# Kernel optimization log

Hardware: AMD Instinct MI355X
Metric: run time of the kernel (lower is better)

The kernel has to match this reference:

```python
import jax, jax.numpy as jnp
import numpy as np

N = 500_000   # total nodes
B = 500       # number of graphs
C = 128       # channels


def setup_inputs() -> dict:
    key = jax.random.key(0)
    ks = jax.random.split(key, 10)
    node_embeddings = jax.random.normal(ks[0], (N, C), dtype=jnp.float32)
    latent_embeddings = jax.random.normal(ks[1], (B, C), dtype=jnp.float32)
    groups = jnp.sort(jax.random.randint(ks[2], (N,), 0, B)).astype(jnp.int32)
    # params (PyTorch Linear stored here as [in, out] matrices; same math)
    s = 1.0 / np.sqrt(C)
    attn_w = jax.random.normal(ks[3], (C, 1), dtype=jnp.float32) * s  # xavier-ish
    w_w = jax.random.normal(ks[4], (C, 1), dtype=jnp.float32) * s
    w_b = jnp.zeros((1,), dtype=jnp.float32)
    f1_w = jax.random.normal(ks[5], (C, C), dtype=jnp.float32) * s
    f1_b = jnp.zeros((C,), dtype=jnp.float32)
    f2_w = jax.random.normal(ks[6], (C, 1), dtype=jnp.float32) * s
    f2_b = jnp.zeros((1,), dtype=jnp.float32)
    return {
        "node_embeddings": node_embeddings,
        "latent_embeddings": latent_embeddings,
        "attn_w": attn_w, "w_w": w_w, "w_b": w_b,
        "f1_w": f1_w, "f1_b": f1_b, "f2_w": f2_w, "f2_b": f2_b,
        "groups": groups, "num_segments": B,
    }


def reference(node_embeddings, latent_embeddings, attn_w, w_w, w_b,
              f1_w, f1_b, f2_w, f2_b, groups, num_segments):
    # gather per-node context (faithful to original: indexes node table by graph id)
    ctx = node_embeddings[groups]            # [N, C]
    lat = latent_embeddings[groups]          # [N, C]
    alpha = jax.nn.sigmoid(ctx @ w_w + w_b)  # [N, 1]
    f_out = jax.nn.relu(lat @ f1_w + f1_b) @ f2_w + f2_b  # [N, 1]
    attn = alpha * f_out + (1.0 - alpha) * attn_w.T       # [N, C]
    scores = jnp.sum(node_embeddings * attn, axis=1, keepdims=True)  # [N, 1]
    scores = jnp.exp(scores - jnp.max(scores, axis=0, keepdims=True))
    denom = jax.ops.segment_sum(scores, groups, num_segments=num_segments)[groups]
    scores = scores / denom
    graph_embeddings = jax.ops.segment_sum(node_embeddings * scores, groups,
                                           num_segments=num_segments)  # [B, C]
    return graph_embeddings
```

## Files before the change

### kernel.cpp

```cpp
#include <hip/hip_runtime.h>
#include <math.h>

#define C 128
#define NW 16

typedef float f32x4 __attribute__((ext_vector_type(4)));

__global__ void k_prep(const int* __restrict__ groups, int n, int b, int nbb,
                       const float* __restrict__ node,
                       const float* __restrict__ latent,
                       const float* __restrict__ attn_w,
                       const float* __restrict__ w_w,
                       const float* __restrict__ w_b,
                       const float* __restrict__ f1_w,
                       const float* __restrict__ f1_b,
                       const float* __restrict__ f2_w,
                       const float* __restrict__ f2_b,
                       int* __restrict__ start, float* __restrict__ attnv) {
    __shared__ float lds_lat[C];
    __shared__ float red[4];

    if ((int)blockIdx.x < nbb) {
        int i = blockIdx.x * blockDim.x + threadIdx.x;
        if (i >= n) return;
        int g = groups[i];
        int gp = (i == 0) ? -1 : groups[i - 1];
        for (int gg = gp + 1; gg <= g; ++gg) start[gg] = i;
        if (i == n - 1)
            for (int gg = g + 1; gg <= b; ++gg) start[gg] = n;
        return;
    }

    const int g = blockIdx.x - nbb;
    const int tid = threadIdx.x;
    const int lane = tid & 63;
    const int wv = tid >> 6;

    if (tid < C) lds_lat[tid] = latent[(size_t)g * C + tid];
    __syncthreads();
    if (tid < C) {
        float ap = node[(size_t)g * C + tid] * w_w[tid];
        float h0 = 0.f, h1 = 0.f;
        #pragma unroll 8
        for (int in = 0; in < C / 2; ++in)
            h0 = fmaf(lds_lat[in], f1_w[in * C + tid], h0);
        #pragma unroll 8
        for (int in = C / 2; in < C; ++in)
            h1 = fmaf(lds_lat[in], f1_w[in * C + tid], h1);
        float h = fmaxf(h0 + h1 + f1_b[tid], 0.f);
        float fp = h * f2_w[tid];
        #pragma unroll
        for (int off = 32; off >= 1; off >>= 1) {
            ap += __shfl_xor(ap, off);
            fp += __shfl_xor(fp, off);
        }
        if (lane == 0) { red[wv * 2] = ap; red[wv * 2 + 1] = fp; }
    }
    __syncthreads();
    if (tid < C) {
        float a_sum = red[0] + red[2];
        float f_sum = red[1] + red[3];
        float alpha = 1.f / (1.f + __expf(-(a_sum + w_b[0])));
        float fout = f_sum + f2_b[0];
        attnv[(size_t)g * C + tid] = alpha * fout + (1.f - alpha) * attn_w[tid];
    }
}

__global__ __launch_bounds__(1024, 8)
void k_attn(const float* __restrict__ node,
            const float* __restrict__ attnv,
            const int* __restrict__ start,
            float* __restrict__ out) {
    const int g = blockIdx.x;
    const int tid = threadIdx.x;
    const int lane = tid & 63;
    const int wv = tid >> 6;

    __shared__ float wacc[NW][C];
    __shared__ float wm[NW], wd[NW];

    const int lo = start[g], hi = start[g + 1];

    const int half = lane >> 5;
    const int cl = lane & 31;
    const f32x4 av = *(const f32x4*)&attnv[(size_t)g * C + cl * 4];

    float m = -INFINITY, denom = 0.f;
    f32x4 acc = (f32x4)(0.f);

    for (int base = lo + wv * 8; base < hi; base += NW * 8) {
        f32x4 r[4];
        #pragma unroll
        for (int j = 0; j < 4; ++j) {
            int row = base + 2 * j + half;
            int rc = row < hi ? row : (hi - 1);
            r[j] = *(const f32x4*)&node[(size_t)rc * C + cl * 4];
        }
        float s[4];
        #pragma unroll
        for (int j = 0; j < 4; ++j)
            s[j] = fmaf(r[j].x, av.x, fmaf(r[j].y, av.y,
                    fmaf(r[j].z, av.z, r[j].w * av.w)));

        float k0, k1;
        {
            float ka = (lane & 1) ? s[1] : s[0];
            float sa = (lane & 1) ? s[0] : s[1];
            float kb = (lane & 1) ? s[3] : s[2];
            float sb = (lane & 1) ? s[2] : s[3];
            k0 = ka + __shfl_xor(sa, 1);
            k1 = kb + __shfl_xor(sb, 1);
        }
        float k;
        {
            float ka = (lane & 2) ? k1 : k0;
            float sa = (lane & 2) ? k0 : k1;
            k = ka + __shfl_xor(sa, 2);
        }
        k += __shfl_xor(k, 4);
        k += __shfl_xor(k, 8);
        k += __shfl_xor(k, 16);
        int rown = base + 2 * (lane & 3) + half;
        k = (rown < hi) ? k : -INFINITY;

        float mx = k;
        mx = fmaxf(mx, __shfl_xor(mx, 1));
        mx = fmaxf(mx, __shfl_xor(mx, 2));
        mx = fmaxf(mx, __shfl_xor(mx, 32));
        float mb = fmaxf(m, mx);
        float scale = __expf(m - mb);
        float p = __expf(k - mb);

        float ps = p;
        ps += __shfl_xor(ps, 1);
        ps += __shfl_xor(ps, 2);
        ps += __shfl_xor(ps, 32);
        denom = fmaf(denom, scale, ps);

        float pe[4], po[4];
        #pragma unroll
        for (int t = 0; t < 4; ++t) {
            pe[t] = __shfl(p, t);
            po[t] = __shfl(p, 32 + t);
        }
        acc.x *= scale; acc.y *= scale; acc.z *= scale; acc.w *= scale;
        #pragma unroll
        for (int j = 0; j < 4; ++j) {
            float pj = half ? po[j] : pe[j];
            acc.x = fmaf(pj, r[j].x, acc.x);
            acc.y = fmaf(pj, r[j].y, acc.y);
            acc.z = fmaf(pj, r[j].z, acc.z);
            acc.w = fmaf(pj, r[j].w, acc.w);
        }
        m = mb;
    }

    acc.x += __shfl_xor(acc.x, 32);
    acc.y += __shfl_xor(acc.y, 32);
    acc.z += __shfl_xor(acc.z, 32);
    acc.w += __shfl_xor(acc.w, 32);

    if (lane == 0) { wm[wv] = m; wd[wv] = denom; }
    if (lane < 32) {
        wacc[wv][cl * 4 + 0] = acc.x;
        wacc[wv][cl * 4 + 1] = acc.y;
        wacc[wv][cl * 4 + 2] = acc.z;
        wacc[wv][cl * 4 + 3] = acc.w;
    }
    __syncthreads();

    if (tid < C) {
        float M = -INFINITY;
        #pragma unroll
        for (int w = 0; w < NW; ++w) M = fmaxf(M, wm[w]);
        float D = 0.f, A = 0.f;
        #pragma unroll
        for (int w = 0; w < NW; ++w) {
            float sc = (wm[w] == -INFINITY) ? 0.f : __expf(wm[w] - M);
            D = fmaf(wd[w], sc, D);
            A = fmaf(wacc[w][tid], sc, A);
        }
        out[(size_t)g * C + tid] = (D > 0.f) ? (A / D) : 0.f;
    }
}

extern "C" void kernel_launch(void* const* d_in, const int* in_sizes, int n_in,
                              void* d_out, int out_size, void* d_ws, size_t ws_size,
                              hipStream_t stream) {
    const float* node   = (const float*)d_in[0];
    const float* latent = (const float*)d_in[1];
    const float* attn_w = (const float*)d_in[2];
    const float* w_w    = (const float*)d_in[3];
    const float* w_b    = (const float*)d_in[4];
    const float* f1_w   = (const float*)d_in[5];
    const float* f1_b   = (const float*)d_in[6];
    const float* f2_w   = (const float*)d_in[7];
    const float* f2_b   = (const float*)d_in[8];
    const int*   groups = (const int*)d_in[9];

    const int n = in_sizes[9];
    const int b = in_sizes[1] / C;

    int*   start = (int*)d_ws;
    float* attnv = (float*)((char*)d_ws + 4096);

    const int nbb = (n + 255) / 256;
    k_prep<<<nbb + b, 256, 0, stream>>>(groups, n, b, nbb, node, latent,
                                        attn_w, w_w, w_b, f1_w, f1_b, f2_w, f2_b,
                                        start, attnv);
    k_attn<<<b, 1024, 0, stream>>>(node, attnv, start, (float*)d_out);
}
```

Measured before the change: 51.00 us.

## Fuse segment-boundary search and attention-vector prep into the attention kernel

Drops the separate prep kernel that scanned the whole groups array to build segment starts and wrote per-graph attention vectors to workspace. Each block now finds its own segment bounds by scanning a window of groups centred on the position it would hold if segments were evenly sized, with a full-array scan as fallback if the window misses. It also computes the small MLP in-block, splitting the 128x128 matvec across all 1024 threads and keeping the attention vector in LDS. This removes one launch and a global round-trip. In exchange every block does extra prologue work before streaming node rows, and the fallback scan is costly if segments are skewed.

```diff
diff --git a/kernel.cpp b/kernel.cpp
--- a/kernel.cpp
+++ b/kernel.cpp
@@ -3,52 +3,89 @@
 
 #define C 128
 #define NW 16
+#define NT 1024
+#define WIN 8192
 
 typedef float f32x4 __attribute__((ext_vector_type(4)));
 
-__global__ void k_prep(const int* __restrict__ groups, int n, int b, int nbb,
-                       const float* __restrict__ node,
-                       const float* __restrict__ latent,
-                       const float* __restrict__ attn_w,
-                       const float* __restrict__ w_w,
-                       const float* __restrict__ w_b,
-                       const float* __restrict__ f1_w,
-                       const float* __restrict__ f1_b,
-                       const float* __restrict__ f2_w,
-                       const float* __restrict__ f2_b,
-                       int* __restrict__ start, float* __restrict__ attnv) {
-    __shared__ float lds_lat[C];
-    __shared__ float red[4];
-
-    if ((int)blockIdx.x < nbb) {
-        int i = blockIdx.x * blockDim.x + threadIdx.x;
-        if (i >= n) return;
-        int g = groups[i];
-        int gp = (i == 0) ? -1 : groups[i - 1];
-        for (int gg = gp + 1; gg <= g; ++gg) start[gg] = i;
-        if (i == n - 1)
-            for (int gg = g + 1; gg <= b; ++gg) start[gg] = n;
-        return;
-    }
-
-    const int g = blockIdx.x - nbb;
+__global__ __launch_bounds__(NT, 8)
+void k_attn(const float* __restrict__ node,
+            const float* __restrict__ latent,
+            const float* __restrict__ attn_w,
+            const float* __restrict__ w_w,
+            const float* __restrict__ w_b,
+            const float* __restrict__ f1_w,
+            const float* __restrict__ f1_b,
+            const float* __restrict__ f2_w,
+            const float* __restrict__ f2_b,
+            const int* __restrict__ groups, int n,
+            float* __restrict__ out) {
+    const int g = blockIdx.x;
+    const int B = gridDim.x;
     const int tid = threadIdx.x;
     const int lane = tid & 63;
     const int wv = tid >> 6;
 
+    __shared__ float lds_attn[C];
+    __shared__ float lds_lat[C];
+    __shared__ float sh_h[8][C];
+    __shared__ float red[4];
+    __shared__ float wacc[NW][C];
+    __shared__ float wm[NW], wd[NW];
+    __shared__ int s_lo, s_hi;
+
+    if (tid == 0) { s_lo = (g == 0) ? 0 : -1; s_hi = (g == B - 1) ? n : -1; }
     if (tid < C) lds_lat[tid] = latent[(size_t)g * C + tid];
     __syncthreads();
+
+    {
+        const int center = g * (n / B) + (n / B) / 2;
+        int wbase = center - WIN / 2;
+        if (wbase < 1) wbase = 1;
+        #pragma unroll
+        for (int k = 0; k < WIN / NT; ++k) {
+            int i = wbase + tid + k * NT;
+            if (i < n) {
+                int gi = groups[i];
+                int gp = groups[i - 1];
+                if (gp < g && g <= gi) s_lo = i;
+                if (gp < g + 1 && g + 1 <= gi) s_hi = i;
+            }
+        }
+    }
+
+    {
+        const int c = tid & (C - 1);
+        const int seg = tid >> 7;
+        float hp = 0.f;
+        #pragma unroll
+        for (int in = seg * 16; in < seg * 16 + 16; ++in)
+            hp = fmaf(lds_lat[in], f1_w[in * C + c], hp);
+        sh_h[seg][c] = hp;
+    }
+    __syncthreads();
+
+    if (s_lo < 0 || s_hi < 0) {
+        for (int i = 1 + tid; i < n; i += NT) {
+            int gi = groups[i];
+            int gp = groups[i - 1];
+            if (gp < g && g <= gi) s_lo = i;
+            if (gp < g + 1 && g + 1 <= gi) s_hi = i;
+        }
+        __syncthreads();
+        if (tid == 0) {
+            if (s_lo < 0) s_lo = (groups[0] >= g) ? 0 : n;
+            if (s_hi < 0) s_hi = (groups[0] >= g + 1) ? 0 : n;
+        }
+    }
+
     if (tid < C) {
+        float h = sh_h[0][tid] + sh_h[1][tid] + sh_h[2][tid] + sh_h[3][tid]
+                + sh_h[4][tid] + sh_h[5][tid] + sh_h[6][tid] + sh_h[7][tid]
+                + f1_b[tid];
+        h = fmaxf(h, 0.f);
+        float fp = h * f2_w[tid];
         float ap = node[(size_t)g * C + tid] * w_w[tid];
-        float h0 = 0.f, h1 = 0.f;
-        #pragma unroll 8
-        for (int in = 0; in < C / 2; ++in)
-            h0 = fmaf(lds_lat[in], f1_w[in * C + tid], h0);
-        #pragma unroll 8
-        for (int in = C / 2; in < C; ++in)
-            h1 = fmaf(lds_lat[in], f1_w[in * C + tid], h1);
-        float h = fmaxf(h0 + h1 + f1_b[tid], 0.f);
-        float fp = h * f2_w[tid];
         #pragma unroll
         for (int off = 32; off >= 1; off >>= 1) {
             ap += __shfl_xor(ap, off);
@@ -62,28 +99,15 @@
         float f_sum = red[1] + red[3];
         float alpha = 1.f / (1.f + __expf(-(a_sum + w_b[0])));
         float fout = f_sum + f2_b[0];
-        attnv[(size_t)g * C + tid] = alpha * fout + (1.f - alpha) * attn_w[tid];
-    }
-}
-
-__global__ __launch_bounds__(1024, 8)
-void k_attn(const float* __restrict__ node,
-            const float* __restrict__ attnv,
-            const int* __restrict__ start,
-            float* __restrict__ out) {
-    const int g = blockIdx.x;
-    const int tid = threadIdx.x;
-    const int lane = tid & 63;
-    const int wv = tid >> 6;
-
-    __shared__ float wacc[NW][C];
-    __shared__ float wm[NW], wd[NW];
-
-    const int lo = start[g], hi = start[g + 1];
+        lds_attn[tid] = alpha * fout + (1.f - alpha) * attn_w[tid];
+    }
+    __syncthreads();
+
+    const int lo = s_lo, hi = s_hi;
 
     const int half = lane >> 5;
     const int cl = lane & 31;
-    const f32x4 av = *(const f32x4*)&attnv[(size_t)g * C + cl * 4];
+    const f32x4 av = *(const f32x4*)&lds_attn[cl * 4];
 
     float m = -INFINITY, denom = 0.f;
     f32x4 acc = (f32x4)(0.f);
@@ -201,12 +225,7 @@
     const int n = in_sizes[9];
     const int b = in_sizes[1] / C;
 
-    int*   start = (int*)d_ws;
-    float* attnv = (float*)((char*)d_ws + 4096);
-
-    const int nbb = (n + 255) / 256;
-    k_prep<<<nbb + b, 256, 0, stream>>>(groups, n, b, nbb, node, latent,
-                                        attn_w, w_w, w_b, f1_w, f1_b, f2_w, f2_b,
-                                        start, attnv);
-    k_attn<<<b, 1024, 0, stream>>>(node, attnv, start, (float*)d_out);
+    k_attn<<<b, NT, 0, stream>>>(node, latent, attn_w, w_w, w_b,
+                                 f1_w, f1_b, f2_w, f2_b, groups, n,
+                                 (float*)d_out);
 }
```

Measured after the change: 47.99 us. -5.9%, faster.
